# Kernel tuning notes

Hardware: AMD Instinct MI355X
Metric: run time of the kernel (lower is better)

## Reference

```python
import jax, jax.numpy as jnp
import numpy as np

N = 100000      # nodes
E = 1200000     # edges per relation
R = 3           # relations
D_IN = 64       # input_dim
HEAD = 4
HD = 16         # output_dim per head
HHD = HEAD * HD # head * output_dim
NEG_SLOPE = 0.01  # torch LeakyReLU default


def setup_inputs() -> dict:
    key = jax.random.key(0)
    ks = jax.random.split(key, 12)
    sc = 0.05
    h = jax.random.normal(ks[0], (N, D_IN), dtype=jnp.float32)
    src = jax.random.randint(ks[1], (R, E), 0, N, dtype=jnp.int32)
    dst = jax.random.randint(ks[2], (R, E), 0, N, dtype=jnp.int32)
    # shared RelationAware d_liner
    d_w = jax.random.normal(ks[3], (D_IN, HHD), dtype=jnp.float32) * sc
    d_b = jnp.zeros((HHD,), jnp.float32)
    # per-relation H_layer w_liner
    w_w = jax.random.normal(ks[4], (R, D_IN, HHD), dtype=jnp.float32) * sc
    w_b = jnp.zeros((R, HHD), jnp.float32)
    # per-relation attention Linear(3*hd, 1)
    atten_w = jax.random.normal(ks[5], (R, 3 * HD), dtype=jnp.float32) * sc
    atten_b = jnp.zeros((R,), jnp.float32)
    # per-relation Gate beta: (2*head*hd, 1)
    beta = jax.random.normal(ks[6], (R, 2 * HHD), dtype=jnp.float32) * sc
    # final combine liner: (R*head*hd -> head*hd)
    lin_w = jax.random.normal(ks[7], (R * HHD, HHD), dtype=jnp.float32) * sc
    lin_b = jnp.zeros((HHD,), jnp.float32)
    return dict(h=h, src=src, dst=dst, d_w=d_w, d_b=d_b, w_w=w_w, w_b=w_b,
                atten_w=atten_w, atten_b=atten_b, beta=beta, lin_w=lin_w, lin_b=lin_b)


def _relation(h, d_feat, s, t, w_w_r, w_b_r, atten_w_r, atten_b_r, beta_r):
    # H_layer forward for one relation; s/t are edge src/dst indices [E]
    hp = h @ w_w_r + w_b_r                       # [N, HHD] (w_liner)
    # RelationAware: tanh(src + dst + (src - dst)) == tanh(2*src)
    es = jnp.tanh(2.0 * d_feat[s])               # [E, HHD] per-edge edge_sum
    src_h = hp[s].reshape(E, HEAD, HD)
    dst_h = hp[t].reshape(E, HEAD, HD)
    es_h = es.reshape(E, HEAD, HD)
    # atten Linear(3*hd,1) on concat[src,dst,edge_s]: split weight, avoid concat
    wa = atten_w_r.reshape(3, HD)
    logits = src_h @ wa[0] + dst_h @ wa[1] + es_h @ wa[2] + atten_b_r  # [E, HEAD]
    alpha = jnp.where(logits >= 0, logits, NEG_SLOPE * logits)          # leaky_relu
    # segment softmax over incoming edges per destination, per head
    amax = jnp.full((N, HEAD), jnp.finfo(jnp.float32).min, jnp.float32).at[t].max(alpha)
    ex = jnp.exp(alpha - amax[t])                                        # [E, HEAD]
    denom = jax.ops.segment_sum(ex, t, num_segments=N)                   # [N, HEAD]
    w = ex / jnp.maximum(denom[t], 1e-20)
    out = jax.ops.segment_sum(w[..., None] * src_h, t, num_segments=N)   # [N, HEAD, HD]
    out = out.reshape(N, HHD)
    # mean of edge_sum over incoming edges per destination
    cnt = jax.ops.segment_sum(jnp.ones((E,), jnp.float32), t, num_segments=N)
    es_node = jax.ops.segment_sum(es, t, num_segments=N) / jnp.maximum(cnt, 1.0)[:, None]
    # Gate
    gate = jax.nn.sigmoid(jnp.concatenate([es_node, out], axis=1) @ beta_r[:, None])  # [N,1]
    return gate * out + (1.0 - gate) * hp


def reference(h, src, dst, d_w, d_b, w_w, w_b, atten_w, atten_b, beta, lin_w, lin_b):
    d_feat = h @ d_w + d_b                        # shared RelationAware d_liner, [N, HHD]
    hs = [
        _relation(h, d_feat, src[r], dst[r], w_w[r], w_b[r], atten_w[r], atten_b[r], beta[r])
        for r in range(R)
    ]
    x = jnp.concatenate(hs, axis=1)               # [N, R*HHD]; dropout p=0 -> identity
    return x @ lin_w + lin_b                      # [N, HHD]
```

## Files before the change

kernel.cpp:

```cpp
#include <hip/hip_runtime.h>

#define N_NODES 100000
#define N_EDGES 1200000
#define R_REL 3
#define RN (R_REL * N_NODES)
#define RE (R_REL * N_EDGES)

#define B_BITS 9
#define W_BKT 512
#define NB_R 196
#define K_BKT (R_REL * NB_R)
#define TILE_A 8192
#define NBLK_A ((RE + TILE_A - 1) / TILE_A)

__device__ __forceinline__ float bcast(float v, int l) {
  return __int_as_float(__builtin_amdgcn_readlane(__float_as_int(v), l));
}

__device__ __forceinline__ int rel_of(int e) {
  return (e >= 2 * N_EDGES) ? 2 : (e >= N_EDGES ? 1 : 0);
}

__global__ void k_zero(int* p, int n) {
  int i = blockIdx.x * 256 + threadIdx.x;
  if (i < n) p[i] = 0;
}

__global__ __launch_bounds__(256) void k_hist(const int* __restrict__ dst,
                                              int* __restrict__ tot) {
  __shared__ int sh[K_BKT];
  int tid = threadIdx.x;
  for (int i = tid; i < K_BKT; i += 256) sh[i] = 0;
  __syncthreads();
  int base = blockIdx.x * TILE_A;
  int end = min(base + TILE_A, RE);
  for (int e = base + tid; e < end; e += 256) {
    atomicAdd(&sh[rel_of(e) * NB_R + (dst[e] >> B_BITS)], 1);
  }
  __syncthreads();
  for (int i = tid; i < K_BKT; i += 256) {
    int c = sh[i];
    if (c) atomicAdd(&tot[i], c);
  }
}

__global__ void k_scanK(const int* __restrict__ tot, int* __restrict__ BB,
                        int* __restrict__ cursor) {
  __shared__ int sd[256];
  int t = threadIdx.x;
  int v[3];
  int tots = 0;
#pragma unroll
  for (int q = 0; q < 3; q++) {
    int k = t * 3 + q;
    v[q] = (k < K_BKT) ? tot[k] : 0;
    tots += v[q];
  }
  sd[t] = tots;
  __syncthreads();
  for (int off = 1; off < 256; off <<= 1) {
    int x = (t >= off) ? sd[t - off] : 0;
    __syncthreads();
    sd[t] += x;
    __syncthreads();
  }
  int run = sd[t] - tots;
#pragma unroll
  for (int q = 0; q < 3; q++) {
    int k = t * 3 + q;
    if (k < K_BKT) {
      BB[k] = run;
      cursor[k] = run;
    }
    run += v[q];
  }
  if (t == 255) BB[K_BKT] = RE;
}

__global__ __launch_bounds__(256) void k_scatterA(const int* __restrict__ src,
                                                  const int* __restrict__ dst,
                                                  int* __restrict__ cursor,
                                                  unsigned int* __restrict__ rec) {
  __shared__ int sh[K_BKT];
  int tid = threadIdx.x;
  for (int i = tid; i < K_BKT; i += 256) sh[i] = 0;
  __syncthreads();
  int base = blockIdx.x * TILE_A;
  int end = min(base + TILE_A, RE);
  for (int e = base + tid; e < end; e += 256) {
    atomicAdd(&sh[rel_of(e) * NB_R + (dst[e] >> B_BITS)], 1);
  }
  __syncthreads();
  for (int i = tid; i < K_BKT; i += 256) {
    int c = sh[i];
    sh[i] = c ? atomicAdd(&cursor[i], c) : 0;
  }
  __syncthreads();
  for (int e = base + tid; e < end; e += 256) {
    int d = dst[e];
    int k = rel_of(e) * NB_R + (d >> B_BITS);
    int p = atomicAdd(&sh[k], 1);
    rec[p] = ((unsigned)src[e] << B_BITS) | (unsigned)(d & (W_BKT - 1));
  }
}

__global__ __launch_bounds__(256) void k_bsort(const unsigned int* __restrict__ rec,
                                               const int* __restrict__ BB,
                                               int* __restrict__ P,
                                               int* __restrict__ ssrc) {
  __shared__ int cnt[W_BKT];
  __shared__ int sd[256];
  int kb = blockIdx.x;
  int r = kb / NB_R;
  int nb0 = (kb % NB_R) * W_BKT;
  int beg = BB[kb], end = BB[kb + 1];
  int tid = threadIdx.x;
  cnt[tid] = 0;
  cnt[256 + tid] = 0;
  __syncthreads();
  for (int e = beg + tid; e < end; e += 256)
    atomicAdd(&cnt[rec[e] & (W_BKT - 1)], 1);
  __syncthreads();
  int v0 = cnt[2 * tid], v1 = cnt[2 * tid + 1];
  int tot2 = v0 + v1;
  sd[tid] = tot2;
  __syncthreads();
  for (int off = 1; off < 256; off <<= 1) {
    int x = (tid >= off) ? sd[tid - off] : 0;
    __syncthreads();
    sd[tid] += x;
    __syncthreads();
  }
  int run = sd[tid] - tot2;
  int node0 = nb0 + 2 * tid;
  int pbase = r * N_NODES + node0;
  if (node0 < N_NODES) P[pbase] = beg + run;
  if (node0 + 1 < N_NODES) P[pbase + 1] = beg + run + v0;
  cnt[2 * tid] = beg + run;
  cnt[2 * tid + 1] = beg + run + v0;
  __syncthreads();
  for (int e = beg + tid; e < end; e += 256) {
    unsigned rc = rec[e];
    int p = atomicAdd(&cnt[rc & (W_BKT - 1)], 1);
    ssrc[p] = (int)(rc >> B_BITS);
  }
}

__global__ __launch_bounds__(256) void k_node(
    const float* __restrict__ h, const float* __restrict__ d_w,
    const float* __restrict__ d_b, const float* __restrict__ w_w,
    const float* __restrict__ w_b, const float* __restrict__ atten_w,
    const float* __restrict__ atten_b, const float* __restrict__ beta,
    float* __restrict__ hp, float* __restrict__ pk, float* __restrict__ adst) {
  __shared__ float sW[4 * 4096];
  int tid = threadIdx.x;
  for (int idx = tid; idx < 4096; idx += 256) {
    sW[idx] = d_w[idx];
    sW[4096 + idx] = w_w[idx];
    sW[8192 + idx] = w_w[4096 + idx];
    sW[12288 + idx] = w_w[8192 + idx];
  }
  __syncthreads();
  int lane = tid & 63, wid = tid >> 6;
  int wave = blockIdx.x * 4 + wid, nw = gridDim.x * 4;
  int k16 = lane & 15, hgrp = lane >> 4;
  float dbv = d_b[lane];
  float wbv0 = w_b[lane], wbv1 = w_b[64 + lane], wbv2 = w_b[128 + lane];
  float wa0[3], wa1[3], wa2[3], ab[3], bb[3];
#pragma unroll
  for (int r = 0; r < 3; r++) {
    wa0[r] = atten_w[r * 48 + k16];
    wa1[r] = atten_w[r * 48 + 16 + k16];
    wa2[r] = atten_w[r * 48 + 32 + k16];
    ab[r] = atten_b[r];
    bb[r] = beta[r * 128 + lane];
  }
  for (int g = wave; g < N_NODES / 8; g += nw) {
    int n0 = g * 8;
    float hr[8];
#pragma unroll
    for (int i = 0; i < 8; i++) hr[i] = h[(n0 + i) * 64 + lane];
    float acc[8][4];
#pragma unroll
    for (int i = 0; i < 8; i++) {
      acc[i][0] = dbv; acc[i][1] = wbv0; acc[i][2] = wbv1; acc[i][3] = wbv2;
    }
#pragma unroll 4
    for (int k = 0; k < 64; k++) {
      float w0 = sW[k * 64 + lane];
      float w1 = sW[4096 + k * 64 + lane];
      float w2 = sW[8192 + k * 64 + lane];
      float w3 = sW[12288 + k * 64 + lane];
#pragma unroll
      for (int i = 0; i < 8; i++) {
        float a = bcast(hr[i], k);
        acc[i][0] += a * w0; acc[i][1] += a * w1;
        acc[i][2] += a * w2; acc[i][3] += a * w3;
      }
    }
#pragma unroll
    for (int i = 0; i < 8; i++) {
      int n = n0 + i;
      float esv = tanhf(2.f * acc[i][0]);
#pragma unroll
      for (int r = 0; r < 3; r++) {
        int idxrn = r * N_NODES + n;
        float hpv = acc[i][1 + r];
        hp[(size_t)idxrn * 64 + lane] = hpv;
        float cs = hpv * wa0[r] + esv * wa2[r];
        float cd = hpv * wa1[r];
#pragma unroll
        for (int m = 1; m < 16; m <<= 1) {
          cs += __shfl_xor(cs, m);
          cd += __shfl_xor(cd, m);
        }
        float sv = esv * bb[r];
#pragma unroll
        for (int m = 1; m < 64; m <<= 1) sv += __shfl_xor(sv, m);
        if (k16 == 0) {
          pk[(size_t)idxrn * 8 + hgrp] = cs + ab[r];
          adst[(size_t)idxrn * 4 + hgrp] = cd;
        }
        if (lane == 0) pk[(size_t)idxrn * 8 + 4] = sv;
      }
    }
  }
}

#define EDGE_BODY(EE, OA, DS, SD)                                        \
  {                                                                      \
    int s_ = ssrc[EE];                                                   \
    int pb_ = s_ * 8;                                                    \
    float av_ = pkr[pb_ + head];                                         \
    float sv_ = pkr[pb_ + 4];                                            \
    float4 hv_ = *reinterpret_cast<const float4*>(&hpr[s_ * 64 + cq]);   \
    float a_ = av_ + adh;                                                \
    a_ = a_ >= 0.f ? a_ : 0.01f * a_;                                    \
    float ex_ = __expf(a_);                                              \
    OA.x += ex_ * hv_.x;                                                 \
    OA.y += ex_ * hv_.y;                                                 \
    OA.z += ex_ * hv_.z;                                                 \
    OA.w += ex_ * hv_.w;                                                 \
    DS += ex_;                                                           \
    SD += sv_;                                                           \
  }

__global__ __launch_bounds__(512) void k_fused(
    const float* __restrict__ hp, const float* __restrict__ pk,
    const float* __restrict__ adst, const int* __restrict__ P,
    const int* __restrict__ ssrc, const float* __restrict__ beta,
    const float* __restrict__ lin_w, const float* __restrict__ lin_b,
    float* __restrict__ out) {
  __shared__ __align__(16) float sLW[64 * 196];
  int tid = threadIdx.x;
  for (int idx = tid; idx < 192 * 64; idx += 512) {
    int j = idx >> 6, c = idx & 63;
    sLW[c * 196 + j] = lin_w[idx];
  }
  __syncthreads();
  int lane = tid & 63, wid = tid >> 6;
  int g = blockIdx.x * 8 + wid;
  int slot = lane >> 4;
  int c16 = lane & 15;
  int cq = c16 * 4;
  int head = c16 >> 2;
  float y0 = lin_b[lane];
  float y[4] = {y0, y0, y0, y0};
  for (int r = 0; r < 3; r++) {
    const float* __restrict__ hpr = hp + (size_t)r * N_NODES * 64;
    const float* __restrict__ pkr = pk + (size_t)r * N_NODES * 8;
    float4 b1v = *reinterpret_cast<const float4*>(&beta[r * 128 + 64 + cq]);
    float4 hr4[4];
#pragma unroll
    for (int i = 0; i < 4; i++) {
      int n = g * 4 + i;
      int idxrn = r * N_NODES + n;
      int beg = P[idxrn];
      int end = (idxrn + 1 < RN) ? P[idxrn + 1] : RE;
      float adh = adst[idxrn * 4 + head];
      float4 hpv = *reinterpret_cast<const float4*>(&hpr[n * 64 + cq]);
      float4 oaA = {0.f, 0.f, 0.f, 0.f}, oaB = {0.f, 0.f, 0.f, 0.f};
      float dsA = 0.f, dsB = 0.f, sdA = 0.f, sdB = 0.f;
      int e = beg + slot;
      for (; e + 4 < end; e += 8) {
        EDGE_BODY(e, oaA, dsA, sdA);
        EDGE_BODY(e + 4, oaB, dsB, sdB);
      }
      if (e < end) EDGE_BODY(e, oaA, dsA, sdA);
      float4 oa;
      oa.x = oaA.x + oaB.x;
      oa.y = oaA.y + oaB.y;
      oa.z = oaA.z + oaB.z;
      oa.w = oaA.w + oaB.w;
      float ds = dsA + dsB, sd = sdA + sdB;
      oa.x += __shfl_xor(oa.x, 16); oa.x += __shfl_xor(oa.x, 32);
      oa.y += __shfl_xor(oa.y, 16); oa.y += __shfl_xor(oa.y, 32);
      oa.z += __shfl_xor(oa.z, 16); oa.z += __shfl_xor(oa.z, 32);
      oa.w += __shfl_xor(oa.w, 16); oa.w += __shfl_xor(oa.w, 32);
      ds += __shfl_xor(ds, 16); ds += __shfl_xor(ds, 32);
      sd += __shfl_xor(sd, 16); sd += __shfl_xor(sd, 32);
      float inv = 1.f / fmaxf(ds, 1e-20f);
      float4 ov;
      ov.x = oa.x * inv; ov.y = oa.y * inv; ov.z = oa.z * inv; ov.w = oa.w * inv;
      float em = sd / fmaxf((float)(end - beg), 1.f);
      float gc = ov.x * b1v.x + ov.y * b1v.y + ov.z * b1v.z + ov.w * b1v.w;
      gc += __shfl_xor(gc, 1); gc += __shfl_xor(gc, 2);
      gc += __shfl_xor(gc, 4); gc += __shfl_xor(gc, 8);
      float gt = 1.f / (1.f + __expf(-(gc + em)));
      float4 hrv;
      hrv.x = gt * ov.x + (1.f - gt) * hpv.x;
      hrv.y = gt * ov.y + (1.f - gt) * hpv.y;
      hrv.z = gt * ov.z + (1.f - gt) * hpv.z;
      hrv.w = gt * ov.w + (1.f - gt) * hpv.w;
      hr4[i] = hrv;
    }
    const float* wrow = &sLW[lane * 196 + r * 64];
#pragma unroll
    for (int j4 = 0; j4 < 64; j4 += 4) {
      float4 wv = *reinterpret_cast<const float4*>(wrow + j4);
      const int sl = j4 >> 2;
#pragma unroll
      for (int i = 0; i < 4; i++) {
        y[i] += bcast(hr4[i].x, sl) * wv.x + bcast(hr4[i].y, sl) * wv.y +
                bcast(hr4[i].z, sl) * wv.z + bcast(hr4[i].w, sl) * wv.w;
      }
    }
  }
#pragma unroll
  for (int i = 0; i < 4; i++) out[(g * 4 + i) * 64 + lane] = y[i];
}

extern "C" void kernel_launch(void* const* d_in, const int* in_sizes, int n_in,
                              void* d_out, int out_size, void* d_ws, size_t ws_size,
                              hipStream_t stream) {
  const float* h = (const float*)d_in[0];
  const int* src = (const int*)d_in[1];
  const int* dst = (const int*)d_in[2];
  const float* d_w = (const float*)d_in[3];
  const float* d_b = (const float*)d_in[4];
  const float* w_w = (const float*)d_in[5];
  const float* w_b = (const float*)d_in[6];
  const float* atten_w = (const float*)d_in[7];
  const float* atten_b = (const float*)d_in[8];
  const float* beta = (const float*)d_in[9];
  const float* lin_w = (const float*)d_in[10];
  const float* lin_b = (const float*)d_in[11];
  float* out = (float*)d_out;

  float* ws = (float*)d_ws;
  float* hp = ws;
  float* pk = hp + (size_t)R_REL * N_NODES * 64;
  float* adst = pk + (size_t)R_REL * N_NODES * 8;
  int* P = (int*)(adst + (size_t)R_REL * N_NODES * 4);
  int* ssrc = P + RN;
  unsigned int* rec = (unsigned int*)(ssrc + RE);
  int* tot = (int*)(rec + RE);
  int* BB = tot + K_BKT;
  int* cursor = BB + K_BKT + 1;

  k_zero<<<(K_BKT + 255) / 256, 256, 0, stream>>>(tot, K_BKT);
  k_hist<<<NBLK_A, 256, 0, stream>>>(dst, tot);
  k_scanK<<<1, 256, 0, stream>>>(tot, BB, cursor);
  k_scatterA<<<NBLK_A, 256, 0, stream>>>(src, dst, cursor, rec);
  k_bsort<<<K_BKT, 256, 0, stream>>>(rec, BB, P, ssrc);
  k_node<<<1024, 256, 0, stream>>>(h, d_w, d_b, w_w, w_b, atten_w, atten_b, beta,
                                   hp, pk, adst);
  k_fused<<<N_NODES / 32, 512, 0, stream>>>(hp, pk, adst, P, ssrc, beta, lin_w,
                                            lin_b, out);
}
```

Measured before the change: 584.3 us.

## Interleave per-node logit and edge-sum, drop LDS lin_w staging, memset counters

The per-node record now stores each head's source logit next to the edge-sum scalar, so each edge gathers one float2 instead of two scattered floats. The fused kernel no longer stages lin_w into a 50KB shared-memory transpose and reads weights directly from global memory (coalesced per lane). Launch bounds now request higher occupancy. The zero kernel is replaced by hipMemsetAsync. Dropping the LDS staging raises occupancy and removes a per-block prologue, but moves the weight reads to the L1/L2 caches.

```diff
diff --git a/kernel.cpp b/kernel.cpp
--- a/kernel.cpp
+++ b/kernel.cpp
@@ -19,11 +19,6 @@
 
 __device__ __forceinline__ int rel_of(int e) {
   return (e >= 2 * N_EDGES) ? 2 : (e >= N_EDGES ? 1 : 0);
-}
-
-__global__ void k_zero(int* p, int n) {
-  int i = blockIdx.x * 256 + threadIdx.x;
-  if (i < n) p[i] = 0;
 }
 
 __global__ __launch_bounds__(256) void k_hist(const int* __restrict__ dst,
@@ -218,10 +213,10 @@
 #pragma unroll
         for (int m = 1; m < 64; m <<= 1) sv += __shfl_xor(sv, m);
         if (k16 == 0) {
-          pk[(size_t)idxrn * 8 + hgrp] = cs + ab[r];
+          float2 rec2 = make_float2(cs + ab[r], sv);
+          *reinterpret_cast<float2*>(&pk[(size_t)idxrn * 8 + hgrp * 2]) = rec2;
           adst[(size_t)idxrn * 4 + hgrp] = cd;
         }
-        if (lane == 0) pk[(size_t)idxrn * 8 + 4] = sv;
       }
     }
   }
@@ -230,11 +225,9 @@
 #define EDGE_BODY(EE, OA, DS, SD)                                        \
   {                                                                      \
     int s_ = ssrc[EE];                                                   \
-    int pb_ = s_ * 8;                                                    \
-    float av_ = pkr[pb_ + head];                                         \
-    float sv_ = pkr[pb_ + 4];                                            \
+    float2 pv_ = *reinterpret_cast<const float2*>(&pkr[s_ * 8 + head2]); \
     float4 hv_ = *reinterpret_cast<const float4*>(&hpr[s_ * 64 + cq]);   \
-    float a_ = av_ + adh;                                                \
+    float a_ = pv_.x + adh;                                              \
     a_ = a_ >= 0.f ? a_ : 0.01f * a_;                                    \
     float ex_ = __expf(a_);                                              \
     OA.x += ex_ * hv_.x;                                                 \
@@ -242,33 +235,29 @@
     OA.z += ex_ * hv_.z;                                                 \
     OA.w += ex_ * hv_.w;                                                 \
     DS += ex_;                                                           \
-    SD += sv_;                                                           \
-  }
-
-__global__ __launch_bounds__(512) void k_fused(
+    SD += pv_.y;                                                         \
+  }
+
+__global__ __launch_bounds__(512, 8) void k_fused(
     const float* __restrict__ hp, const float* __restrict__ pk,
     const float* __restrict__ adst, const int* __restrict__ P,
     const int* __restrict__ ssrc, const float* __restrict__ beta,
     const float* __restrict__ lin_w, const float* __restrict__ lin_b,
     float* __restrict__ out) {
-  __shared__ __align__(16) float sLW[64 * 196];
-  int tid = threadIdx.x;
-  for (int idx = tid; idx < 192 * 64; idx += 512) {
-    int j = idx >> 6, c = idx & 63;
-    sLW[c * 196 + j] = lin_w[idx];
-  }
-  __syncthreads();
+  int tid = threadIdx.x;
   int lane = tid & 63, wid = tid >> 6;
   int g = blockIdx.x * 8 + wid;
   int slot = lane >> 4;
   int c16 = lane & 15;
   int cq = c16 * 4;
   int head = c16 >> 2;
+  int head2 = head * 2;
   float y0 = lin_b[lane];
   float y[4] = {y0, y0, y0, y0};
   for (int r = 0; r < 3; r++) {
     const float* __restrict__ hpr = hp + (size_t)r * N_NODES * 64;
     const float* __restrict__ pkr = pk + (size_t)r * N_NODES * 8;
+    const float* __restrict__ lwr = lin_w + r * 64 * 64;
     float4 b1v = *reinterpret_cast<const float4*>(&beta[r * 128 + 64 + cq]);
     float4 hr4[4];
 #pragma unroll
@@ -314,15 +303,17 @@
       hrv.w = gt * ov.w + (1.f - gt) * hpv.w;
       hr4[i] = hrv;
     }
-    const float* wrow = &sLW[lane * 196 + r * 64];
 #pragma unroll
     for (int j4 = 0; j4 < 64; j4 += 4) {
-      float4 wv = *reinterpret_cast<const float4*>(wrow + j4);
+      float w0 = lwr[(j4 + 0) * 64 + lane];
+      float w1 = lwr[(j4 + 1) * 64 + lane];
+      float w2 = lwr[(j4 + 2) * 64 + lane];
+      float w3 = lwr[(j4 + 3) * 64 + lane];
       const int sl = j4 >> 2;
 #pragma unroll
       for (int i = 0; i < 4; i++) {
-        y[i] += bcast(hr4[i].x, sl) * wv.x + bcast(hr4[i].y, sl) * wv.y +
-                bcast(hr4[i].z, sl) * wv.z + bcast(hr4[i].w, sl) * wv.w;
+        y[i] += bcast(hr4[i].x, sl) * w0 + bcast(hr4[i].y, sl) * w1 +
+                bcast(hr4[i].z, sl) * w2 + bcast(hr4[i].w, sl) * w3;
       }
     }
   }
@@ -358,7 +349,7 @@
   int* BB = tot + K_BKT;
   int* cursor = BB + K_BKT + 1;
 
-  k_zero<<<(K_BKT + 255) / 256, 256, 0, stream>>>(tot, K_BKT);
+  hipMemsetAsync(tot, 0, K_BKT * sizeof(int), stream);
   k_hist<<<NBLK_A, 256, 0, stream>>>(dst, tot);
   k_scanK<<<1, 256, 0, stream>>>(tot, BB, cursor);
   k_scatterA<<<NBLK_A, 256, 0, stream>>>(src, dst, cursor, rec);
```

New measurement: 923.6 us. 1.58x slower.
